# Kernel tuning notes

Measured on AMD Instinct MI355X. Metric: run time of the kernel, lower is better.

The kernel has to match this reference:

```python
import jax, jax.numpy as jnp
import numpy as np


def setup_inputs() -> dict:
    key = jax.random.key(0)
    ks = jax.random.split(key, 8)
    B, C, P1, P2 = 8, 256, 2048, 4096
    Cq = C // 8
    return {
        "x1": jax.random.normal(ks[0], (B, C, P1), dtype=jnp.float32),
        "x2": jax.random.normal(ks[1], (B, C, P2), dtype=jnp.float32),
        "Wq": jax.random.normal(ks[2], (Cq, C), dtype=jnp.float32) * (1.0 / np.sqrt(C)),
        "bq": jnp.zeros((Cq,), dtype=jnp.float32),
        "Wk": jax.random.normal(ks[3], (Cq, C), dtype=jnp.float32) * (1.0 / np.sqrt(C)),
        "bk": jnp.zeros((Cq,), dtype=jnp.float32),
        "Wv": jax.random.normal(ks[4], (C, C), dtype=jnp.float32) * (1.0 / np.sqrt(C)),
        "bv": jnp.zeros((C,), dtype=jnp.float32),
        "alpha": jnp.ones((1,), dtype=jnp.float32),
    }


def reference(x1, x2, Wq, bq, Wk, bk, Wv, bv, alpha):
    # Conv1d(kernel_size=1) == pointwise linear over channel dim.
    # q: [B, P1, Cq]   (Q(x1) then permute(0,2,1))
    q = jnp.einsum('oc,bcp->bpo', Wq, x1) + bq[None, None, :]
    # k: [B, Cq, P2]
    k = jnp.einsum('oc,bcp->bop', Wk, x2) + bk[None, :, None]
    # v: [B, C, P1]
    v = jnp.einsum('oc,bcp->bop', Wv, x1) + bv[None, :, None]
    # energy: [B, P1, P2]; unscaled attention, softmax over P2
    energy = jnp.einsum('bpo,boq->bpq', q, k)
    attention = jax.nn.softmax(energy, axis=-1)
    # out: [B, C, P2]
    out = jnp.einsum('bcp,bpq->bcq', v, attention)
    return alpha * out + x2
```

## Files before the change

kernel.cpp:

```cpp
#include <hip/hip_runtime.h>

#define B 8
#define C 256
#define P1 2048
#define P2 4096
#define CQ 32

typedef _Float16 h8 __attribute__((ext_vector_type(8)));
typedef _Float16 h4 __attribute__((ext_vector_type(4)));
typedef float f4 __attribute__((ext_vector_type(4)));

#define MFMA16(a, b, c) __builtin_amdgcn_mfma_f32_16x16x32_f16(a, b, c, 0, 0, 0)

__global__ void prep_w(const float* __restrict__ Wq, const float* __restrict__ Wk,
                       const float* __restrict__ Wv,
                       _Float16* __restrict__ Wqh, _Float16* __restrict__ Wql,
                       _Float16* __restrict__ Wkh, _Float16* __restrict__ Wkl,
                       _Float16* __restrict__ Wvh) {
    const int i = blockIdx.x * 256 + threadIdx.x;
    if (i < CQ * C) {
        float a = Wq[i]; _Float16 h = (_Float16)a;
        Wqh[i] = h; Wql[i] = (_Float16)(a - (float)h);
        float b2 = Wk[i]; _Float16 h2 = (_Float16)b2;
        Wkh[i] = h2; Wkl[i] = (_Float16)(b2 - (float)h2);
    }
    for (int j = i; j < C * C; j += 32 * 256)
        Wvh[j] = (_Float16)Wv[j];
}

__global__ __launch_bounds__(256) void prep1(
        const float* __restrict__ x1,
        const _Float16* __restrict__ Wqh, const _Float16* __restrict__ Wql,
        const _Float16* __restrict__ Wvh,
        const float* __restrict__ bq, const float* __restrict__ bv,
        _Float16* __restrict__ qhw, _Float16* __restrict__ qlw,
        _Float16* __restrict__ vhw) {
    __shared__ float xs[32][257];
    const int t  = threadIdx.x;
    const int b  = blockIdx.x;
    const int p0 = blockIdx.y * 32;
    const float* xb = x1 + (size_t)b * C * P1;

    {
        const int pl = t & 31, cg = t >> 5;
#pragma unroll 8
        for (int i = 0; i < 32; ++i) {
            int c = cg * 32 + i;
            xs[pl][c] = xb[(size_t)c * P1 + p0 + pl];
        }
    }
    __syncthreads();

    const int w = t >> 6, lane = t & 63, ln = lane & 15, quad = lane >> 4;
    const int nh = w & 1, ch = w >> 1;
    const int prow = nh * 16 + ln;

    f4 accv[8];
#pragma unroll
    for (int mt = 0; mt < 8; ++mt) accv[mt] = (f4){0.f, 0.f, 0.f, 0.f};
    f4 accq = {0.f, 0.f, 0.f, 0.f};

    for (int ks = 0; ks < 8; ++ks) {
        const int c0 = ks * 32 + quad * 8;
        h8 bh, bl;
#pragma unroll
        for (int j = 0; j < 8; ++j) {
            float xv = xs[prow][c0 + j];
            _Float16 hh = (_Float16)xv;
            bh[j] = hh; bl[j] = (_Float16)(xv - (float)hh);
        }
#pragma unroll
        for (int mt = 0; mt < 8; ++mt) {
            h8 a = *(const h8*)&Wvh[(size_t)((ch * 8 + mt) * 16 + ln) * C + c0];
            accv[mt] = MFMA16(a, bh, accv[mt]);
            accv[mt] = MFMA16(a, bl, accv[mt]);
        }
        {
            h8 aqh = *(const h8*)&Wqh[(size_t)(ch * 16 + ln) * C + c0];
            h8 aql = *(const h8*)&Wql[(size_t)(ch * 16 + ln) * C + c0];
            accq = MFMA16(aql, bh, accq);
            accq = MFMA16(aqh, bl, accq);
            accq = MFMA16(aqh, bh, accq);
        }
    }

#pragma unroll
    for (int mt = 0; mt < 8; ++mt) {
        int cb = (ch * 8 + mt) * 16 + quad * 4;
        f4 bvv = *(const f4*)&bv[cb];
#pragma unroll
        for (int r = 0; r < 4; ++r)
            vhw[((size_t)b * C + cb + r) * P1 + p0 + prow] =
                (_Float16)(accv[mt][r] + bvv[r]);
    }
    {
        int ob = ch * 16 + quad * 4;
        f4 bqv = *(const f4*)&bq[ob];
        h4 hv, lv;
#pragma unroll
        for (int r = 0; r < 4; ++r) {
            float val = accq[r] + bqv[r];
            _Float16 hh = (_Float16)val;
            hv[r] = hh; lv[r] = (_Float16)(val - (float)hh);
        }
        size_t row = ((size_t)b * P1 + p0 + prow) * CQ + ob;
        *(h4*)(qhw + row) = hv;
        *(h4*)(qlw + row) = lv;
    }
}

__global__ __launch_bounds__(256) void prep2(
        const float* __restrict__ x2,
        const _Float16* __restrict__ Wkh, const _Float16* __restrict__ Wkl,
        const float* __restrict__ bk,
        _Float16* __restrict__ khw, _Float16* __restrict__ klw) {
    __shared__ float xs[32][257];
    const int t  = threadIdx.x;
    const int b  = blockIdx.x;
    const int p0 = blockIdx.y * 32;
    const float* xb = x2 + (size_t)b * C * P2;
    {
        const int pl = t & 31, cg = t >> 5;
#pragma unroll 8
        for (int i = 0; i < 32; ++i) {
            int c = cg * 32 + i;
            xs[pl][c] = xb[(size_t)c * P2 + p0 + pl];
        }
    }
    __syncthreads();

    const int w = t >> 6, lane = t & 63, ln = lane & 15, quad = lane >> 4;
    const int nh = w & 1, mh = w >> 1;
    const int prow = nh * 16 + ln;

    f4 accq = {0.f, 0.f, 0.f, 0.f};
    for (int ks = 0; ks < 8; ++ks) {
        const int c0 = ks * 32 + quad * 8;
        h8 bh, bl;
#pragma unroll
        for (int j = 0; j < 8; ++j) {
            float xv = xs[prow][c0 + j];
            _Float16 hh = (_Float16)xv;
            bh[j] = hh; bl[j] = (_Float16)(xv - (float)hh);
        }
        h8 akh = *(const h8*)&Wkh[(size_t)(mh * 16 + ln) * C + c0];
        h8 akl = *(const h8*)&Wkl[(size_t)(mh * 16 + ln) * C + c0];
        accq = MFMA16(akl, bh, accq);
        accq = MFMA16(akh, bl, accq);
        accq = MFMA16(akh, bh, accq);
    }
    {
        int ob = mh * 16 + quad * 4;
        f4 bkv = *(const f4*)&bk[ob];
        h4 hv, lv;
#pragma unroll
        for (int r = 0; r < 4; ++r) {
            float val = accq[r] + bkv[r];
            _Float16 hh = (_Float16)val;
            hv[r] = hh; lv[r] = (_Float16)(val - (float)hh);
        }
        size_t row = ((size_t)b * P2 + p0 + prow) * CQ + ob;
        *(h4*)(khw + row) = hv;
        *(h4*)(klw + row) = lv;
    }
}

__global__ __launch_bounds__(512) void stats_l(
        const _Float16* __restrict__ qhi, const _Float16* __restrict__ qlo,
        const _Float16* __restrict__ khi, const _Float16* __restrict__ klo,
        float* __restrict__ linv) {
    __shared__ float lred[4][32];
    const int t = threadIdx.x;
    const int b = blockIdx.x;
    const int p0 = blockIdx.y * 32;
    const int w = t >> 6, lane = t & 63, ln = lane & 15, quad = lane >> 4;
    const int ptw = w & 1, qq = w >> 1;
    const int pbase = p0 + ptw * 16;

    h8 qh = *(const h8*)(qhi + ((size_t)b * P1 + pbase + ln) * CQ + quad * 8);
    h8 ql = *(const h8*)(qlo + ((size_t)b * P1 + pbase + ln) * CQ + quad * 8);

    const _Float16* khb = khi + (size_t)b * P2 * CQ;
    const _Float16* klb = klo + (size_t)b * P2 * CQ;
    const int base = qq * 1024;

    h8 kh0 = *(const h8*)(khb + (size_t)(base + ln) * CQ + quad * 8);
    h8 kl0 = *(const h8*)(klb + (size_t)(base + ln) * CQ + quad * 8);
    h8 kh1 = *(const h8*)(khb + (size_t)(base + 16 + ln) * CQ + quad * 8);
    h8 kl1 = *(const h8*)(klb + (size_t)(base + 16 + ln) * CQ + quad * 8);

    f4 acc = {0.f, 0.f, 0.f, 0.f};
    for (int ti = 0; ti < 64; ti += 2) {
        h8 ch0 = kh0, cl0 = kl0, ch1 = kh1, cl1 = kl1;
        if (ti + 2 < 64) {
            int q2 = base + (ti + 2) * 16 + ln;
            kh0 = *(const h8*)(khb + (size_t)q2 * CQ + quad * 8);
            kl0 = *(const h8*)(klb + (size_t)q2 * CQ + quad * 8);
            kh1 = *(const h8*)(khb + (size_t)(q2 + 16) * CQ + quad * 8);
            kl1 = *(const h8*)(klb + (size_t)(q2 + 16) * CQ + quad * 8);
        }
        f4 z = {0.f, 0.f, 0.f, 0.f};
        f4 e0 = MFMA16(ql, ch0, z);
        e0 = MFMA16(qh, cl0, e0);
        e0 = MFMA16(qh, ch0, e0);
        f4 e1 = MFMA16(ql, ch1, z);
        e1 = MFMA16(qh, cl1, e1);
        e1 = MFMA16(qh, ch1, e1);
#pragma unroll
        for (int r = 0; r < 4; ++r)
            acc[r] += __expf(e0[r]) + __expf(e1[r]);
    }
#pragma unroll
    for (int off = 1; off < 16; off <<= 1) {
#pragma unroll
        for (int r = 0; r < 4; ++r) acc[r] += __shfl_xor(acc[r], off);
    }
    if (ln == 0) *(f4*)&lred[qq][ptw * 16 + quad * 4] = acc;
    __syncthreads();
    if (t < 32)
        linv[(size_t)b * P1 + p0 + t] =
            1.0f / (lred[0][t] + lred[1][t] + lred[2][t] + lred[3][t]);
}

__global__ __launch_bounds__(512)
__attribute__((amdgpu_waves_per_eu(4, 4)))
void attn_gemm(
        const _Float16* __restrict__ qhi, const _Float16* __restrict__ qlo,
        const _Float16* __restrict__ khi, const _Float16* __restrict__ klo,
        const _Float16* __restrict__ vhi, const float* __restrict__ linv,
        const float* __restrict__ x2, const float* __restrict__ alpha_p,
        float* __restrict__ out) {
    __shared__ _Float16 att_s[2][64][256];

    const int t  = threadIdx.x;
    const int b  = blockIdx.x & 7;
    const int q0 = (blockIdx.x >> 3) * 64;
    const int w  = t >> 6;
    const int lane = t & 63, ln = lane & 15, quad = lane >> 4;
    const int sw = ln & 7;

    h8 kh[4], kl[4];
#pragma unroll
    for (int nt = 0; nt < 4; ++nt) {
        int q = q0 + nt * 16 + ln;
        kh[nt] = *(const h8*)(khi + ((size_t)b * P2 + q) * CQ + quad * 8);
        kl[nt] = *(const h8*)(klo + ((size_t)b * P2 + q) * CQ + quad * 8);
    }

    f4 acc[2][4];
#pragma unroll
    for (int mt = 0; mt < 2; ++mt)
#pragma unroll
        for (int nt = 0; nt < 4; ++nt) acc[mt][nt] = (f4){0.f, 0.f, 0.f, 0.f};

    const _Float16* vrow0 = vhi + ((size_t)b * C + w * 32 + ln) * P1;
    const _Float16* vrow1 = vrow0 + (size_t)16 * P1;

    h8 avc[2];
    avc[0] = *(const h8*)(vrow0 + quad * 8);
    avc[1] = *(const h8*)(vrow1 + quad * 8);

    h8 nqh[2], nql[2];
#pragma unroll
    for (int pt = 0; pt < 2; ++pt) {
        size_t r = ((size_t)b * P1 + pt * 128 + w * 16 + ln) * CQ + quad * 8;
        nqh[pt] = *(const h8*)(qhi + r);
        nql[pt] = *(const h8*)(qlo + r);
    }

    for (int pc = 0; pc < P1 / 256; ++pc) {
        const int p0v = pc * 256;
        h8 cqh0 = nqh[0], cql0 = nql[0], cqh1 = nqh[1], cql1 = nql[1];

        _Float16* abuf = &att_s[pc & 1][0][0];
#pragma unroll
        for (int pt = 0; pt < 2; ++pt) {
            h8 cqh = pt ? cqh1 : cqh0;
            h8 cql = pt ? cql1 : cql0;
            f4 lv = *(const f4*)(linv + (size_t)b * P1 + p0v + pt * 128
                                 + w * 16 + quad * 4);
            const int gb = (pt << 4) + (w << 1) + (quad >> 1);
            const int col = (((gb ^ sw) << 3)) + ((quad & 1) << 2);
#pragma unroll
            for (int nt = 0; nt < 4; ++nt) {
                f4 z = {0.f, 0.f, 0.f, 0.f};
                f4 e = MFMA16(cql, kh[nt], z);
                e = MFMA16(cqh, kl[nt], e);
                e = MFMA16(cqh, kh[nt], e);
                h4 pk;
#pragma unroll
                for (int r = 0; r < 4; ++r)
                    pk[r] = (_Float16)(__expf(e[r]) * lv[r]);
                *(h4*)&abuf[(nt * 16 + ln) * 256 + col] = pk;
            }
        }
        __syncthreads();

        if (pc + 1 < P1 / 256) {
#pragma unroll
            for (int pt = 0; pt < 2; ++pt) {
                size_t r = ((size_t)b * P1 + p0v + 256 + pt * 128
                            + w * 16 + ln) * CQ + quad * 8;
                nqh[pt] = *(const h8*)(qhi + r);
                nql[pt] = *(const h8*)(qlo + r);
            }
        }

#pragma unroll
        for (int kk = 0; kk < 8; ++kk) {
            h8 avn[2];
            {
                int pnext = p0v + (kk + 1) * 32;
                if (pnext < P1) {
                    avn[0] = *(const h8*)(vrow0 + pnext + quad * 8);
                    avn[1] = *(const h8*)(vrow1 + pnext + quad * 8);
                } else {
                    avn[0] = avc[0]; avn[1] = avc[1];
                }
            }
            h8 bf[4];
#pragma unroll
            for (int nt = 0; nt < 4; ++nt) {
                int g = kk * 4 + quad;
                bf[nt] = *(const h8*)&abuf[(nt * 16 + ln) * 256 + ((g ^ sw) << 3)];
            }
            __builtin_amdgcn_s_setprio(1);
#pragma unroll
            for (int mt = 0; mt < 2; ++mt)
#pragma unroll
                for (int nt = 0; nt < 4; ++nt)
                    acc[mt][nt] = MFMA16(avc[mt], bf[nt], acc[mt][nt]);
            __builtin_amdgcn_s_setprio(0);
            avc[0] = avn[0]; avc[1] = avn[1];
        }
    }

    const float alpha = alpha_p[0];
#pragma unroll
    for (int mt = 0; mt < 2; ++mt) {
#pragma unroll
        for (int nt = 0; nt < 4; ++nt) {
            int q = q0 + nt * 16 + ln;
#pragma unroll
            for (int r = 0; r < 4; ++r) {
                int c = w * 32 + mt * 16 + quad * 4 + r;
                size_t o = ((size_t)b * C + c) * P2 + q;
                out[o] = fmaf(alpha, acc[mt][nt][r], x2[o]);
            }
        }
    }
}

extern "C" void kernel_launch(void* const* d_in, const int* in_sizes, int n_in,
                              void* d_out, int out_size, void* d_ws, size_t ws_size,
                              hipStream_t stream) {
    const float* x1    = (const float*)d_in[0];
    const float* x2    = (const float*)d_in[1];
    const float* Wq    = (const float*)d_in[2];
    const float* bq    = (const float*)d_in[3];
    const float* Wk    = (const float*)d_in[4];
    const float* bk    = (const float*)d_in[5];
    const float* Wv    = (const float*)d_in[6];
    const float* bv    = (const float*)d_in[7];
    const float* alpha = (const float*)d_in[8];
    float* out = (float*)d_out;

    _Float16* qh = (_Float16*)d_ws;
    _Float16* ql = qh + (size_t)B * P1 * CQ;
    _Float16* kh = ql + (size_t)B * P1 * CQ;
    _Float16* kl = kh + (size_t)B * P2 * CQ;
    _Float16* vh = kl + (size_t)B * P2 * CQ;
    _Float16* wqh = vh + (size_t)B * C * P1;
    _Float16* wql = wqh + CQ * C;
    _Float16* wkh = wql + CQ * C;
    _Float16* wkl = wkh + CQ * C;
    _Float16* wvh = wkl + CQ * C;
    float*    li  = (float*)(wvh + C * C);

    prep_w<<<dim3(32), 256, 0, stream>>>(Wq, Wk, Wv, wqh, wql, wkh, wkl, wvh);
    prep1<<<dim3(B, P1 / 32), 256, 0, stream>>>(x1, wqh, wql, wvh, bq, bv, qh, ql, vh);
    prep2<<<dim3(B, P2 / 32), 256, 0, stream>>>(x2, wkh, wkl, bk, kh, kl);
    stats_l<<<dim3(B, P1 / 32), 512, 0, stream>>>(qh, ql, kh, kl, li);
    attn_gemm<<<dim3(512), 512, 0, stream>>>(qh, ql, kh, kl, vh, li, x2, alpha, out);
}
```

Measured before the change: 260.9 us.

## Merge Q/V and K projection kernels, vectorize loads, drop V register prefetch

Merges the two projection kernels into one launch whose grid covers both the x1 and x2 column ranges, branching on block index. The global load into shared memory now uses float4 vector reads instead of scalar ones. In the attention GEMM, the software-pipelined V register prefetch is removed in favor of direct per-iteration loads, and the waves_per_eu attribute is replaced by a launch_bounds min-blocks hint. These aim to cut launch overhead and load instruction count, at the risk of exposing V load latency and changing register allocation in the main kernel.

```diff
diff --git a/kernel.cpp b/kernel.cpp
--- a/kernel.cpp
+++ b/kernel.cpp
@@ -28,25 +28,33 @@
         Wvh[j] = (_Float16)Wv[j];
 }
 
-__global__ __launch_bounds__(256) void prep1(
-        const float* __restrict__ x1,
+__global__ __launch_bounds__(256) void prep_qkv(
+        const float* __restrict__ x1, const float* __restrict__ x2,
         const _Float16* __restrict__ Wqh, const _Float16* __restrict__ Wql,
         const _Float16* __restrict__ Wvh,
+        const _Float16* __restrict__ Wkh, const _Float16* __restrict__ Wkl,
         const float* __restrict__ bq, const float* __restrict__ bv,
+        const float* __restrict__ bk,
         _Float16* __restrict__ qhw, _Float16* __restrict__ qlw,
-        _Float16* __restrict__ vhw) {
+        _Float16* __restrict__ vhw,
+        _Float16* __restrict__ khw, _Float16* __restrict__ klw) {
     __shared__ float xs[32][257];
-    const int t  = threadIdx.x;
-    const int b  = blockIdx.x;
-    const int p0 = blockIdx.y * 32;
-    const float* xb = x1 + (size_t)b * C * P1;
+    const int t = threadIdx.x;
+    const int b = blockIdx.x;
+    const int y = blockIdx.y;
+    const bool is1 = (y < P1 / 32);
+    const int p0 = (is1 ? y : y - P1 / 32) * 32;
+    const float* xb = is1 ? x1 + (size_t)b * C * P1 : x2 + (size_t)b * C * P2;
+    const int ps = is1 ? P1 : P2;
 
     {
-        const int pl = t & 31, cg = t >> 5;
-#pragma unroll 8
-        for (int i = 0; i < 32; ++i) {
-            int c = cg * 32 + i;
-            xs[pl][c] = xb[(size_t)c * P1 + p0 + pl];
+        const int pl4 = t & 7, cb = t >> 3;
+#pragma unroll
+        for (int i = 0; i < 8; ++i) {
+            const int c = cb + i * 32;
+            f4 v = *(const f4*)&xb[(size_t)c * ps + p0 + pl4 * 4];
+#pragma unroll
+            for (int r = 0; r < 4; ++r) xs[pl4 * 4 + r][c] = v[r];
         }
     }
     __syncthreads();
@@ -55,113 +63,89 @@
     const int nh = w & 1, ch = w >> 1;
     const int prow = nh * 16 + ln;
 
-    f4 accv[8];
-#pragma unroll
-    for (int mt = 0; mt < 8; ++mt) accv[mt] = (f4){0.f, 0.f, 0.f, 0.f};
-    f4 accq = {0.f, 0.f, 0.f, 0.f};
-
-    for (int ks = 0; ks < 8; ++ks) {
-        const int c0 = ks * 32 + quad * 8;
-        h8 bh, bl;
-#pragma unroll
-        for (int j = 0; j < 8; ++j) {
-            float xv = xs[prow][c0 + j];
-            _Float16 hh = (_Float16)xv;
-            bh[j] = hh; bl[j] = (_Float16)(xv - (float)hh);
+    if (is1) {
+        f4 accv[8];
+#pragma unroll
+        for (int mt = 0; mt < 8; ++mt) accv[mt] = (f4){0.f, 0.f, 0.f, 0.f};
+        f4 accq = {0.f, 0.f, 0.f, 0.f};
+
+        for (int ks = 0; ks < 8; ++ks) {
+            const int c0 = ks * 32 + quad * 8;
+            h8 bh, bl;
+#pragma unroll
+            for (int j = 0; j < 8; ++j) {
+                float xv = xs[prow][c0 + j];
+                _Float16 hh = (_Float16)xv;
+                bh[j] = hh; bl[j] = (_Float16)(xv - (float)hh);
+            }
+#pragma unroll
+            for (int mt = 0; mt < 8; ++mt) {
+                h8 a = *(const h8*)&Wvh[(size_t)((ch * 8 + mt) * 16 + ln) * C + c0];
+                accv[mt] = MFMA16(a, bh, accv[mt]);
+                accv[mt] = MFMA16(a, bl, accv[mt]);
+            }
+            {
+                h8 aqh = *(const h8*)&Wqh[(size_t)(ch * 16 + ln) * C + c0];
+                h8 aql = *(const h8*)&Wql[(size_t)(ch * 16 + ln) * C + c0];
+                accq = MFMA16(aql, bh, accq);
+                accq = MFMA16(aqh, bl, accq);
+                accq = MFMA16(aqh, bh, accq);
+            }
         }
 #pragma unroll
         for (int mt = 0; mt < 8; ++mt) {
-            h8 a = *(const h8*)&Wvh[(size_t)((ch * 8 + mt) * 16 + ln) * C + c0];
-            accv[mt] = MFMA16(a, bh, accv[mt]);
-            accv[mt] = MFMA16(a, bl, accv[mt]);
+            int cb2 = (ch * 8 + mt) * 16 + quad * 4;
+            f4 bvv = *(const f4*)&bv[cb2];
+#pragma unroll
+            for (int r = 0; r < 4; ++r)
+                vhw[((size_t)b * C + cb2 + r) * P1 + p0 + prow] =
+                    (_Float16)(accv[mt][r] + bvv[r]);
         }
         {
-            h8 aqh = *(const h8*)&Wqh[(size_t)(ch * 16 + ln) * C + c0];
-            h8 aql = *(const h8*)&Wql[(size_t)(ch * 16 + ln) * C + c0];
-            accq = MFMA16(aql, bh, accq);
-            accq = MFMA16(aqh, bl, accq);
-            accq = MFMA16(aqh, bh, accq);
-        }
-    }
-
-#pragma unroll
-    for (int mt = 0; mt < 8; ++mt) {
-        int cb = (ch * 8 + mt) * 16 + quad * 4;
-        f4 bvv = *(const f4*)&bv[cb];
-#pragma unroll
-        for (int r = 0; r < 4; ++r)
-            vhw[((size_t)b * C + cb + r) * P1 + p0 + prow] =
-                (_Float16)(accv[mt][r] + bvv[r]);
-    }
-    {
-        int ob = ch * 16 + quad * 4;
-        f4 bqv = *(const f4*)&bq[ob];
-        h4 hv, lv;
-#pragma unroll
-        for (int r = 0; r < 4; ++r) {
-            float val = accq[r] + bqv[r];
-            _Float16 hh = (_Float16)val;
-            hv[r] = hh; lv[r] = (_Float16)(val - (float)hh);
-        }
-        size_t row = ((size_t)b * P1 + p0 + prow) * CQ + ob;
-        *(h4*)(qhw + row) = hv;
-        *(h4*)(qlw + row) = lv;
-    }
-}
-
-__global__ __launch_bounds__(256) void prep2(
-        const float* __restrict__ x2,
-        const _Float16* __restrict__ Wkh, const _Float16* __restrict__ Wkl,
-        const float* __restrict__ bk,
-        _Float16* __restrict__ khw, _Float16* __restrict__ klw) {
-    __shared__ float xs[32][257];
-    const int t  = threadIdx.x;
-    const int b  = blockIdx.x;
-    const int p0 = blockIdx.y * 32;
-    const float* xb = x2 + (size_t)b * C * P2;
-    {
-        const int pl = t & 31, cg = t >> 5;
-#pragma unroll 8
-        for (int i = 0; i < 32; ++i) {
-            int c = cg * 32 + i;
-            xs[pl][c] = xb[(size_t)c * P2 + p0 + pl];
-        }
-    }
-    __syncthreads();
-
-    const int w = t >> 6, lane = t & 63, ln = lane & 15, quad = lane >> 4;
-    const int nh = w & 1, mh = w >> 1;
-    const int prow = nh * 16 + ln;
-
-    f4 accq = {0.f, 0.f, 0.f, 0.f};
-    for (int ks = 0; ks < 8; ++ks) {
-        const int c0 = ks * 32 + quad * 8;
-        h8 bh, bl;
-#pragma unroll
-        for (int j = 0; j < 8; ++j) {
-            float xv = xs[prow][c0 + j];
-            _Float16 hh = (_Float16)xv;
-            bh[j] = hh; bl[j] = (_Float16)(xv - (float)hh);
-        }
-        h8 akh = *(const h8*)&Wkh[(size_t)(mh * 16 + ln) * C + c0];
-        h8 akl = *(const h8*)&Wkl[(size_t)(mh * 16 + ln) * C + c0];
-        accq = MFMA16(akl, bh, accq);
-        accq = MFMA16(akh, bl, accq);
-        accq = MFMA16(akh, bh, accq);
-    }
-    {
-        int ob = mh * 16 + quad * 4;
-        f4 bkv = *(const f4*)&bk[ob];
-        h4 hv, lv;
-#pragma unroll
-        for (int r = 0; r < 4; ++r) {
-            float val = accq[r] + bkv[r];
-            _Float16 hh = (_Float16)val;
-            hv[r] = hh; lv[r] = (_Float16)(val - (float)hh);
-        }
-        size_t row = ((size_t)b * P2 + p0 + prow) * CQ + ob;
-        *(h4*)(khw + row) = hv;
-        *(h4*)(klw + row) = lv;
+            int ob = ch * 16 + quad * 4;
+            f4 bqv = *(const f4*)&bq[ob];
+            h4 hv, lv;
+#pragma unroll
+            for (int r = 0; r < 4; ++r) {
+                float val = accq[r] + bqv[r];
+                _Float16 hh = (_Float16)val;
+                hv[r] = hh; lv[r] = (_Float16)(val - (float)hh);
+            }
+            size_t row = ((size_t)b * P1 + p0 + prow) * CQ + ob;
+            *(h4*)(qhw + row) = hv;
+            *(h4*)(qlw + row) = lv;
+        }
+    } else {
+        f4 accq = {0.f, 0.f, 0.f, 0.f};
+        for (int ks = 0; ks < 8; ++ks) {
+            const int c0 = ks * 32 + quad * 8;
+            h8 bh, bl;
+#pragma unroll
+            for (int j = 0; j < 8; ++j) {
+                float xv = xs[prow][c0 + j];
+                _Float16 hh = (_Float16)xv;
+                bh[j] = hh; bl[j] = (_Float16)(xv - (float)hh);
+            }
+            h8 akh = *(const h8*)&Wkh[(size_t)(ch * 16 + ln) * C + c0];
+            h8 akl = *(const h8*)&Wkl[(size_t)(ch * 16 + ln) * C + c0];
+            accq = MFMA16(akl, bh, accq);
+            accq = MFMA16(akh, bl, accq);
+            accq = MFMA16(akh, bh, accq);
+        }
+        {
+            int ob = ch * 16 + quad * 4;
+            f4 bkv = *(const f4*)&bk[ob];
+            h4 hv, lv;
+#pragma unroll
+            for (int r = 0; r < 4; ++r) {
+                float val = accq[r] + bkv[r];
+                _Float16 hh = (_Float16)val;
+                hv[r] = hh; lv[r] = (_Float16)(val - (float)hh);
+            }
+            size_t row = ((size_t)b * P2 + p0 + prow) * CQ + ob;
+            *(h4*)(khw + row) = hv;
+            *(h4*)(klw + row) = lv;
+        }
     }
 }
 
@@ -222,9 +206,7 @@
             1.0f / (lred[0][t] + lred[1][t] + lred[2][t] + lred[3][t]);
 }
 
-__global__ __launch_bounds__(512)
-__attribute__((amdgpu_waves_per_eu(4, 4)))
-void attn_gemm(
+__global__ __launch_bounds__(512, 4) void attn_gemm(
         const _Float16* __restrict__ qhi, const _Float16* __restrict__ qlo,
         const _Float16* __restrict__ khi, const _Float16* __restrict__ klo,
         const _Float16* __restrict__ vhi, const float* __restrict__ linv,
@@ -256,10 +238,6 @@
     const _Float16* vrow0 = vhi + ((size_t)b * C + w * 32 + ln) * P1;
     const _Float16* vrow1 = vrow0 + (size_t)16 * P1;
 
-    h8 avc[2];
-    avc[0] = *(const h8*)(vrow0 + quad * 8);
-    avc[1] = *(const h8*)(vrow1 + quad * 8);
-
     h8 nqh[2], nql[2];
 #pragma unroll
     for (int pt = 0; pt < 2; ++pt) {
@@ -270,17 +248,15 @@
 
     for (int pc = 0; pc < P1 / 256; ++pc) {
         const int p0v = pc * 256;
-        h8 cqh0 = nqh[0], cql0 = nql[0], cqh1 = nqh[1], cql1 = nql[1];
-
         _Float16* abuf = &att_s[pc & 1][0][0];
+
 #pragma unroll
         for (int pt = 0; pt < 2; ++pt) {
-            h8 cqh = pt ? cqh1 : cqh0;
-            h8 cql = pt ? cql1 : cql0;
+            h8 cqh = nqh[pt], cql = nql[pt];
             f4 lv = *(const f4*)(linv + (size_t)b * P1 + p0v + pt * 128
                                  + w * 16 + quad * 4);
             const int gb = (pt << 4) + (w << 1) + (quad >> 1);
-            const int col = (((gb ^ sw) << 3)) + ((quad & 1) << 2);
+            const int col = ((gb ^ sw) << 3) + ((quad & 1) << 2);
 #pragma unroll
             for (int nt = 0; nt < 4; ++nt) {
                 f4 z = {0.f, 0.f, 0.f, 0.f};
@@ -308,30 +284,22 @@
 
 #pragma unroll
         for (int kk = 0; kk < 8; ++kk) {
-            h8 avn[2];
-            {
-                int pnext = p0v + (kk + 1) * 32;
-                if (pnext < P1) {
-                    avn[0] = *(const h8*)(vrow0 + pnext + quad * 8);
-                    avn[1] = *(const h8*)(vrow1 + pnext + quad * 8);
-                } else {
-                    avn[0] = avc[0]; avn[1] = avc[1];
-                }
-            }
             h8 bf[4];
 #pragma unroll
             for (int nt = 0; nt < 4; ++nt) {
                 int g = kk * 4 + quad;
                 bf[nt] = *(const h8*)&abuf[(nt * 16 + ln) * 256 + ((g ^ sw) << 3)];
             }
+            h8 av0 = *(const h8*)(vrow0 + p0v + kk * 32 + quad * 8);
+            h8 av1 = *(const h8*)(vrow1 + p0v + kk * 32 + quad * 8);
             __builtin_amdgcn_s_setprio(1);
 #pragma unroll
-            for (int mt = 0; mt < 2; ++mt)
-#pragma unroll
-                for (int nt = 0; nt < 4; ++nt)
-                    acc[mt][nt] = MFMA16(avc[mt], bf[nt], acc[mt][nt]);
+            for (int nt = 0; nt < 4; ++nt)
+                acc[0][nt] = MFMA16(av0, bf[nt], acc[0][nt]);
+#pragma unroll
+            for (int nt = 0; nt < 4; ++nt)
+                acc[1][nt] = MFMA16(av1, bf[nt], acc[1][nt]);
             __builtin_amdgcn_s_setprio(0);
-            avc[0] = avn[0]; avc[1] = avn[1];
         }
     }
 
@@ -378,8 +346,8 @@
     float*    li  = (float*)(wvh + C * C);
 
     prep_w<<<dim3(32), 256, 0, stream>>>(Wq, Wk, Wv, wqh, wql, wkh, wkl, wvh);
-    prep1<<<dim3(B, P1 / 32), 256, 0, stream>>>(x1, wqh, wql, wvh, bq, bv, qh, ql, vh);
-    prep2<<<dim3(B, P2 / 32), 256, 0, stream>>>(x2, wkh, wkl, bk, kh, kl);
+    prep_qkv<<<dim3(B, P1 / 32 + P2 / 32), 256, 0, stream>>>(
+        x1, x2, wqh, wql, wvh, wkh, wkl, bq, bv, bk, qh, ql, vh, kh, kl);
     stats_l<<<dim3(B, P1 / 32), 512, 0, stream>>>(qh, ql, kh, kl, li);
     attn_gemm<<<dim3(512), 512, 0, stream>>>(qh, ql, kh, kl, vh, li, x2, alpha, out);
 }
```

Measured after the change: 246.2 us. 1.06x faster.
